# Optimization experiments

Hardware: AMD Instinct MI355X
Metric: run time of the kernel (lower is better)

## Reference

```python
import jax, jax.numpy as jnp
import numpy as np

NEG = -1e9  # large negative for masked logits (TRT uses dtype min)

def _rotate_every_two(x):
    # pairs (x0,x1) -> (-x1, x0), interleaved along last dim
    xr = x.reshape(*x.shape[:-1], -1, 2)
    rot = jnp.stack([-xr[..., 1], xr[..., 0]], axis=-1)
    return rot.reshape(x.shape)

def _apply_rope(x, cos, sin):
    # rot_dim == cos.shape[-1]; here it equals the full inner dim
    rot_dim = cos.shape[-1]
    x_rot, x_pass = x[..., :rot_dim], x[..., rot_dim:]
    x_rot = x_rot * cos + _rotate_every_two(x_rot) * sin
    return jnp.concatenate([x_rot, x_pass], axis=-1) if x_pass.shape[-1] else x_rot

def setup_inputs() -> dict:
    key = jax.random.key(0)
    ks = jax.random.split(key, 12)
    B, N, D_MODEL, H, DH = 2, 2048, 1024, 16, 64
    INNER = H * DH
    x = jax.random.normal(ks[0], (B, N, D_MODEL), dtype=jnp.float32)
    # rope angles: build realistic cos/sin tables repeated per head
    pos = jnp.arange(N, dtype=jnp.float32)
    inv = 1.0 / (10000.0 ** (jnp.arange(0, DH, 2, dtype=jnp.float32) / DH))
    ang = pos[:, None] * inv[None, :]              # [N, DH/2]
    ang = jnp.repeat(ang, 2, axis=-1)              # [N, DH] interleaved pairs
    ang = jnp.tile(ang, (1, H))                    # [N, INNER]
    rope_cos = jnp.broadcast_to(jnp.cos(ang)[None], (B, N, INNER)).astype(jnp.float32)
    rope_sin = jnp.broadcast_to(jnp.sin(ang)[None], (B, N, INNER)).astype(jnp.float32)
    input_lengths = jax.random.randint(ks[1], (B,), N // 2, N + 1, dtype=jnp.int32)
    s = 1.0 / np.sqrt(D_MODEL)
    Wq = jax.random.normal(ks[2], (D_MODEL, INNER), dtype=jnp.float32) * s
    bq = jnp.zeros((INNER,), jnp.float32)
    Wk = jax.random.normal(ks[3], (D_MODEL, INNER), dtype=jnp.float32) * s
    bk = jnp.zeros((INNER,), jnp.float32)
    Wv = jax.random.normal(ks[4], (D_MODEL, INNER), dtype=jnp.float32) * s
    bv = jnp.zeros((INNER,), jnp.float32)
    Wo = jax.random.normal(ks[5], (INNER, D_MODEL), dtype=jnp.float32) * (1.0 / np.sqrt(INNER))
    bo = jnp.zeros((D_MODEL,), jnp.float32)
    return {"x": x, "rope_cos": rope_cos, "rope_sin": rope_sin,
            "input_lengths": input_lengths,
            "Wq": Wq, "bq": bq, "Wk": Wk, "bk": bk, "Wv": Wv, "bv": bv,
            "Wo": Wo, "bo": bo}

def reference(x, rope_cos, rope_sin, input_lengths, Wq, bq, Wk, bk, Wv, bv, Wo, bo):
    B, N, _ = x.shape
    H, DH = 16, 64
    q = x @ Wq + bq
    k = x @ Wk + bk
    v = x @ Wv + bv
    q = _apply_rope(q, rope_cos, rope_sin)
    k = _apply_rope(k, rope_cos, rope_sin)
    # split heads: [B,N,H,DH] -> [B,H,N,DH]
    q = q.reshape(B, N, H, DH).transpose(0, 2, 1, 3)
    k = k.reshape(B, N, H, DH).transpose(0, 2, 1, 3)
    v = v.reshape(B, N, H, DH).transpose(0, 2, 1, 3)
    # NOTE: faithful to the non-plugin source path, q is NOT pre-scaled
    scores = jnp.einsum('bhqd,bhkd->bhqk', q, k)
    key_mask = jnp.arange(N)[None, :] < input_lengths[:, None]  # [B,N]
    scores = scores + jnp.where(key_mask, 0.0, NEG).astype(scores.dtype)[:, None, None, :]
    probs = jax.nn.softmax(scores, axis=-1)
    ctx = jnp.einsum('bhqk,bhkd->bhqd', probs, v)  # [B,H,N,DH]
    ctx = ctx.transpose(0, 2, 1, 3).reshape(B, N, H * DH)
    out = ctx @ Wo + bo
    out = out * key_mask[..., None].astype(out.dtype)
    return out
```

## Files before the change

kernel.cpp:

```cpp
#include <hip/hip_runtime.h>
#include <hip/hip_bf16.h>


typedef __fp16 fp16x2 __attribute__((ext_vector_type(2)));
typedef _Float16 f16x8 __attribute__((ext_vector_type(8)));
typedef float f32x4 __attribute__((ext_vector_type(4)));
typedef float f32x16 __attribute__((ext_vector_type(16)));

#define NEGBIG (-1.0e9f)

__device__ inline f32x4 mfma16(f16x8 a, f16x8 b, f32x4 c) {
  return __builtin_amdgcn_mfma_f32_16x16x32_f16(a, b, c, 0, 0, 0);
}
__device__ inline f32x16 mfma32(f16x8 a, f16x8 b, f32x16 c) {
  return __builtin_amdgcn_mfma_f32_32x32x16_f16(a, b, c, 0, 0, 0);
}

__device__ inline void gload16(const void* g, void* l) {
  __builtin_amdgcn_global_load_lds(
      (const __attribute__((address_space(1))) void*)g,
      (__attribute__((address_space(3))) void*)l, 16, 0, 0);
}

__device__ inline unsigned pk2u(float a, float b) {
  union { fp16x2 h; unsigned u; } x;
  x.h = __builtin_amdgcn_cvt_pkrtz(a, b);
  return x.u;
}

__device__ inline float max3f(float a, float b, float c) {
  float d;
  asm("v_max3_f32 %0, %1, %2, %3" : "=v"(d) : "v"(a), "v"(b), "v"(c));
  return d;
}

__global__ __launch_bounds__(256) void prep_kernel(
    const float* __restrict__ x, const float* __restrict__ Wq,
    const float* __restrict__ Wk, const float* __restrict__ Wv,
    const float* __restrict__ Wo, const float* __restrict__ rc,
    const float* __restrict__ rs, _Float16* __restrict__ xh,
    _Float16* __restrict__ wt, float* __restrict__ rc2,
    float* __restrict__ rs2) {
  __shared__ float tile[32][33];
  const int z = blockIdx.z;
  const int tx = threadIdx.x, ty = threadIdx.y;
  if (z == 4) {
    const int bid = blockIdx.y * 32 + blockIdx.x;
    const int t = ty * 32 + tx;
#pragma unroll
    for (int i = 0; i < 4; ++i) {
      const int o = bid * 1024 + i * 256 + t;
      const float4 v = ((const float4*)x)[o];
      union { _Float16 h[4]; short4 s; } u;
      u.h[0] = (_Float16)v.x; u.h[1] = (_Float16)v.y;
      u.h[2] = (_Float16)v.z; u.h[3] = (_Float16)v.w;
      ((short4*)xh)[o] = u.s;
    }
    return;
  }
  if (z == 5) {
    const int bid = blockIdx.y * 32 + blockIdx.x;
    const int idx = bid * 256 + ty * 32 + tx;
    if (idx < 131072) {
      const int n = idx >> 6, d = idx & 63;
      rc2[idx] = rc[(size_t)n * 1024 + d];
      rs2[idx] = rs[(size_t)n * 1024 + d];
    }
    return;
  }
  const float* W = (z == 0) ? Wq : (z == 1) ? Wk : (z == 2) ? Wv : Wo;
  _Float16* dh = wt + (size_t)z * 1024 * 1024;
  const int j0 = blockIdx.x * 32, k0 = blockIdx.y * 32;
  for (int i = ty; i < 32; i += 8)
    tile[i][tx] = W[(size_t)(k0 + i) * 1024 + j0 + tx];
  __syncthreads();
  for (int i = ty; i < 32; i += 8)
    dh[(size_t)(j0 + i) * 1024 + k0 + tx] = (_Float16)tile[tx][i];
}

template <int TM, int EPI>
__global__ __launch_bounds__(256) void gemm_kernel(
    const _Float16* __restrict__ A, const _Float16* __restrict__ B,
    const float* __restrict__ bias0, const float* __restrict__ bias1,
    const float* __restrict__ bias2,
    const float* __restrict__ ropeC, const float* __restrict__ ropeS,
    const int* __restrict__ lens,
    _Float16* __restrict__ outQK, _Float16* __restrict__ outVT,
    float* __restrict__ outF) {
  constexpr int MI = TM / 32;
  constexpr int MSHIFT = (TM == 128) ? 5 : 6;
  __shared__ __align__(16) _Float16 smem[(TM + 128) * 32];
  const int t = threadIdx.x;
  const int w = t >> 6, lane = t & 63;
  const int wr = w >> 1, wc = w & 1;
  const int fr = lane & 15, fg = lane >> 4;
  const int nwg = gridDim.x;
  const int bid = blockIdx.x;
  const int wgid = (bid & 7) * (nwg >> 3) + (bid >> 3);
  const int mtile = wgid & ((1 << MSHIFT) - 1);
  const int ntile = wgid >> MSHIFT;

  const int srow = t >> 2;
  const int skel = (t & 3) << 3;
  const size_t aBase = (size_t)(mtile * TM + srow) * 1024 + skel;
  const size_t bBase = (size_t)(ntile * 128 + srow) * 1024 + skel;
  const int ldst = t * 8;
  _Float16* lA = &smem[0];
  _Float16* lB = &smem[TM * 32];

  f32x4 acc[MI][4];
#pragma unroll
  for (int i = 0; i < MI; ++i)
#pragma unroll
    for (int j = 0; j < 4; ++j) {
      acc[i][j][0] = 0.f; acc[i][j][1] = 0.f; acc[i][j][2] = 0.f; acc[i][j][3] = 0.f;
    }

  for (int k0 = 0; k0 < 1024; k0 += 32) {
    gload16(A + aBase + k0, lA + ldst);
    if constexpr (TM == 128) gload16(A + aBase + k0 + 64 * 1024, lA + ldst + 2048);
    gload16(B + bBase + k0, lB + ldst);
    gload16(B + bBase + k0 + 64 * 1024, lB + ldst + 2048);
    __syncthreads();

    f16x8 af[MI], bf[4];
#pragma unroll
    for (int mi = 0; mi < MI; ++mi)
      af[mi] = *(const f16x8*)&lA[(wr * (TM / 2) + mi * 16 + fr) * 32 + fg * 8];
#pragma unroll
    for (int ni = 0; ni < 4; ++ni)
      bf[ni] = *(const f16x8*)&lB[(wc * 64 + ni * 16 + fr) * 32 + fg * 8];
#pragma unroll
    for (int mi = 0; mi < MI; ++mi)
#pragma unroll
      for (int ni = 0; ni < 4; ++ni)
        acc[mi][ni] = mfma16(af[mi], bf[ni], acc[mi][ni]);
    __syncthreads();
  }

  const int rowbase = mtile * TM + wr * (TM / 2);
  const int colbase = ntile * 128 + wc * 64;

  if constexpr (EPI == 0) {
    const int which = colbase >> 10;
    if (which < 2) {
      const float* bias = which ? bias1 : bias0;
      const int hh = (colbase >> 6) & 15;
      const int b = rowbase >> 11;
      const int nbase = rowbase & 2047;
      _Float16* lslab = smem + w * 1152;
      const char* cslab = (const char*)lslab;
      _Float16* qkbase =
          outQK + (size_t)((which * 2 + b) * 16 + hh) * 2048 * 64;
      const int rrow = lane >> 2;
      const int rqo = (lane & 3) * 32;
#pragma unroll
      for (int mi = 0; mi < MI; ++mi) {
#pragma unroll
        for (int ni = 0; ni < 4; ++ni) {
          const int dd = ni * 16 + fr;
          const float bv = bias[hh * 64 + dd];
#pragma unroll
          for (int r = 0; r < 4; ++r) {
            const int n = nbase + mi * 16 + fg * 4 + r;
            float val = acc[mi][ni][r] + bv;
            float part = __shfl_xor(val, 1);
            const int ro = n * 64 + dd;
            const float c = ropeC[ro], s = ropeS[ro];
            float rot = (fr & 1) ? (val * c + part * s) : (val * c - part * s);
            if (!which) rot *= 1.44269504f;
            lslab[(fg * 4 + r) * 72 + dd] = (_Float16)rot;
          }
        }
        asm volatile("" ::: "memory");
        const uint4 v0 = *(const uint4*)(cslab + rrow * 144 + rqo);
        const uint4 v1 = *(const uint4*)(cslab + rrow * 144 + rqo + 16);
        _Float16* gdst =
            qkbase + (size_t)(nbase + mi * 16 + rrow) * 64 + (lane & 3) * 16;
        *(uint4*)gdst = v0;
        *(uint4*)(gdst + 8) = v1;
        asm volatile("" ::: "memory");
      }
    } else {
#pragma unroll
      for (int ni = 0; ni < 4; ++ni) {
        const int gcol = colbase + ni * 16 + fr;
        const int jj = gcol & 1023;
        const int hh = jj >> 6, dd = jj & 63;
        const float bv = bias2[jj];
#pragma unroll
        for (int mi = 0; mi < MI; ++mi) {
          const int n0 = rowbase + mi * 16 + fg * 4;
          const int b = n0 >> 11, n = n0 & 2047;
          union { _Float16 h[4]; short4 s4; } u;
#pragma unroll
          for (int r = 0; r < 4; ++r) u.h[r] = (_Float16)(acc[mi][ni][r] + bv);
          *(short4*)(outVT + ((size_t)(b * 16 + hh) * 64 + dd) * 2048 + n) = u.s4;
        }
      }
    }
  } else {
    const int b = rowbase >> 11;
    const int len = lens[b];
#pragma unroll
    for (int ni = 0; ni < 4; ++ni) {
      const int gcol = colbase + ni * 16 + fr;
      const float bv = bias0[gcol];
#pragma unroll
      for (int mi = 0; mi < MI; ++mi) {
#pragma unroll
        for (int r = 0; r < 4; ++r) {
          const int m = rowbase + mi * 16 + fg * 4 + r;
          const int n = m & 2047;
          float val = acc[mi][ni][r] + bv;
          if (n >= len) val = 0.f;
          outF[(size_t)m * 1024 + gcol] = val;
        }
      }
    }
  }
}

__global__ __launch_bounds__(256, 4) void attn_kernel(
    const _Float16* __restrict__ qk, const _Float16* __restrict__ vt,
    const int* __restrict__ lens, unsigned* __restrict__ po,
    float2* __restrict__ ml) {
  __shared__ __align__(16) char lds[32768];
  const int t = threadIdx.x;
  const int w = t >> 6, lane = t & 63;
  const int lq = lane & 31, hi = lane >> 5;
  const int gid = blockIdx.x;
  const int xcd = gid & 7, idx = gid >> 3;
  const int qtile = idx & 15;
  const int c = ((idx >> 4) << 3) + xcd;
  const int bh = c >> 2, seg = c & 3;
  const int b = bh >> 4, h = bh & 15;
  const int len = lens[b];
  const int q0w = qtile * 128 + w * 32;
  const size_t qoff = (size_t)(b * 16 + h) * 2048 * 64;
  const size_t koff = (size_t)((2 + b) * 16 + h) * 2048 * 64;
  const size_t voff = (size_t)(b * 16 + h) * 64 * 2048;

  f16x8 qf[4];
#pragma unroll
  for (int ks = 0; ks < 4; ++ks)
    qf[ks] = *(const f16x8*)(qk + qoff + (size_t)(q0w + lq) * 64 + ks * 16 + hi * 8);

  const int srow = t >> 3;
  const int ss = (t & 7) ^ (srow & 7);
  const size_t kg = koff + (size_t)srow * 64 + ss * 8;
  const int vd = srow + ((ss >> 2) << 5);
  const size_t vg = voff + (size_t)vd * 2048 + (ss & 3) * 8;

  f32x16 o0, o1;
#pragma unroll
  for (int i = 0; i < 16; ++i) { o0[i] = 0.f; o1[i] = 0.f; }
  float mrun = 0.f, lsum = 0.f;

  fp16x2 ones2;
  ones2[0] = (__fp16)1.0f; ones2[1] = (__fp16)1.0f;

#define STAGE(bi, tile0) do { \
    char* dst = lds + (bi) * 16384 + t * 16; \
    const size_t kk = (size_t)(tile0) * 2048;  \
    gload16(qk + kg + kk, dst); \
    gload16(qk + kg + kk + 2048, dst + 4096); \
    gload16(vt + vg + (tile0) * 32, dst + 8192); \
    gload16(vt + vg + (tile0) * 32 + 32, dst + 12288); \
  } while (0)

  const int nkb = (len + 31) >> 5;
  const int tb0 = (nkb * seg) >> 2;
  const int tb1 = (nkb * (seg + 1)) >> 2;
  const int nst = (tb1 - tb0 + 1) >> 1;

  STAGE(0, tb0);

  for (int st = 0; st < nst; ++st) {
    const int cur = st & 1;
    if (st + 1 < nst) {
      STAGE(cur ^ 1, tb0 + (st + 1) * 2);
      asm volatile("s_waitcnt vmcnt(4)" ::: "memory");
    } else {
      asm volatile("s_waitcnt vmcnt(0)" ::: "memory");
    }
    __builtin_amdgcn_s_barrier();

    const char* Bb = lds + cur * 16384;
    const int rsw = (lq & 7) << 4;

#pragma unroll
    for (int ch = 0; ch < 2; ++ch) {
      const int kb = tb0 + st * 2 + ch;
      if (kb < tb1) {
        const char* Kb = Bb + ch * 4096;
        const char* Vb = Bb + 8192 + ch * 4096;

        f32x16 s0;
        const float nm = -mrun;
#pragma unroll
        for (int i = 0; i < 16; ++i) s0[i] = nm;
        __builtin_amdgcn_s_setprio(1);
#pragma unroll
        for (int ks = 0; ks < 4; ++ks) {
          const f16x8 kf =
              *(const f16x8*)(Kb + lq * 128 + ((ks * 32 + hi * 16) ^ rsw));
          s0 = mfma32(kf, qf[ks], s0);
        }
        __builtin_amdgcn_s_setprio(0);

        if (kb == nkb - 1 && (len & 31)) {
#pragma unroll
          for (int r = 0; r < 16; ++r) {
            const int key = kb * 32 + (r & 3) + ((r >> 2) << 3) + hi * 4;
            if (key >= len) s0[r] = NEGBIG;
          }
        }

        const float m0 = max3f(s0[0], s0[1], s0[2]);
        const float m1 = max3f(s0[3], s0[4], s0[5]);
        const float m2 = max3f(s0[6], s0[7], s0[8]);
        const float m3 = max3f(s0[9], s0[10], s0[11]);
        const float m4 = max3f(s0[12], s0[13], s0[14]);
        float mx = fmaxf(max3f(m0, m1, m2), max3f(m3, m4, s0[15]));
        mx = fmaxf(mx, __shfl_xor(mx, 32));

        const bool first = (kb == tb0);
        if (first || !__all(mx <= 8.f)) {
          const float delta = first ? mx : fmaxf(mx, 0.f);
          const float scq = __builtin_amdgcn_exp2f(-delta);
          mrun += delta;
          lsum *= scq;
          float sc[16];
#pragma unroll
          for (int r = 0; r < 16; ++r)
            sc[r] = __shfl(scq, (r & 3) + ((r >> 2) << 3) + hi * 4);
#pragma unroll
          for (int r = 0; r < 16; ++r) { o0[r] *= sc[r]; o1[r] *= sc[r]; }
#pragma unroll
          for (int i = 0; i < 16; ++i) s0[i] -= delta;
        }

        unsigned W[8];
#pragma unroll
        for (int u = 0; u < 4; ++u) {
          const float p0 = __builtin_amdgcn_exp2f(s0[4 * u + 0]);
          const float p1 = __builtin_amdgcn_exp2f(s0[4 * u + 1]);
          const float p2 = __builtin_amdgcn_exp2f(s0[4 * u + 2]);
          const float p3 = __builtin_amdgcn_exp2f(s0[4 * u + 3]);
          W[2 * u] = pk2u(p0, p1);
          W[2 * u + 1] = pk2u(p2, p3);
        }
        float ps = 0.f;
#pragma unroll
        for (int i = 0; i < 8; ++i) {
          union { unsigned u; fp16x2 h; } x; x.u = W[i];
          ps = __builtin_amdgcn_fdot2(x.h, ones2, ps, false);
        }
        ps += __shfl_xor(ps, 32);
        lsum += ps;

        __builtin_amdgcn_s_setprio(1);
#pragma unroll
        for (int ks = 0; ks < 2; ++ks) {
          const unsigned w0 = W[4 * ks + 0], w1 = W[4 * ks + 1];
          const unsigned w2 = W[4 * ks + 2], w3 = W[4 * ks + 3];
          const unsigned sendA = hi ? w0 : w2;
          const unsigned sendB = hi ? w1 : w3;
          const unsigned recvA = __shfl_xor(sendA, 32);
          const unsigned recvB = __shfl_xor(sendB, 32);
          union { unsigned u[4]; f16x8 v; } af;
          af.u[0] = hi ? recvA : w0;
          af.u[1] = hi ? recvB : w1;
          af.u[2] = hi ? w2 : recvA;
          af.u[3] = hi ? w3 : recvB;
          const int g0 = ks * 2 + hi;
          const f16x8 v0f = *(const f16x8*)(Vb + lq * 128 + ((g0 << 4) ^ rsw));
          const f16x8 v1f =
              *(const f16x8*)(Vb + lq * 128 + (((g0 + 4) << 4) ^ rsw));
          o0 = mfma32(af.v, v0f, o0);
          o1 = mfma32(af.v, v1f, o1);
        }
        __builtin_amdgcn_s_setprio(0);
      }
    }

    asm volatile("" ::: "memory");
    __builtin_amdgcn_s_barrier();
  }
#undef STAGE

  const size_t rowbase = (size_t)bh * 2048 + q0w;
  const float li = 1.f / lsum;
  unsigned* pod = po + ((size_t)seg * 65536 + rowbase) * 32;
#pragma unroll
  for (int r = 0; r < 16; ++r) {
    const int qr = (r & 3) + ((r >> 2) << 3) + hi * 4;
    const float lr = __shfl(li, qr);
    pod[qr * 32 + lq] = pk2u(o0[r] * lr, o1[r] * lr);
  }
  if (hi == 0) {
    float2 v; v.x = mrun; v.y = lsum;
    ml[(size_t)seg * 65536 + rowbase + lq] = v;
  }
}

__global__ __launch_bounds__(256) void combine_kernel(
    const unsigned* __restrict__ po, const float2* __restrict__ ml,
    _Float16* __restrict__ ctx) {
  const int tid = blockIdx.x * 256 + threadIdx.x;
  const int row = tid >> 5, dg = tid & 31;
  const float2 a0 = ml[row];
  const float2 a1 = ml[65536 + row];
  const float2 a2 = ml[131072 + row];
  const float2 a3 = ml[196608 + row];
  const float m = fmaxf(fmaxf(a0.x, a1.x), fmaxf(a2.x, a3.x));
  const float w0 = a0.y * __builtin_amdgcn_exp2f(a0.x - m);
  const float w1 = a1.y * __builtin_amdgcn_exp2f(a1.x - m);
  const float w2 = a2.y * __builtin_amdgcn_exp2f(a2.x - m);
  const float w3 = a3.y * __builtin_amdgcn_exp2f(a3.x - m);
  const float inv = 1.f / (w0 + w1 + w2 + w3);
  float acc0 = 0.f, acc1 = 0.f;
  const float f[4] = {w0 * inv, w1 * inv, w2 * inv, w3 * inv};
#pragma unroll
  for (int s = 0; s < 4; ++s) {
    union { unsigned u; fp16x2 h; } x;
    x.u = po[((size_t)s * 65536 + row) * 32 + dg];
    acc0 += f[s] * (float)x.h[0];
    acc1 += f[s] * (float)x.h[1];
  }
  const int bh = row >> 11, n = row & 2047, b = bh >> 4, h = bh & 15;
  _Float16* dst = ctx + ((size_t)(b * 2048 + n) * 1024 + h * 64);
  dst[dg] = (_Float16)acc0;
  dst[dg + 32] = (_Float16)acc1;
}


extern "C" void kernel_launch(void* const* d_in, const int* in_sizes, int n_in,
                              void* d_out, int out_size, void* d_ws, size_t ws_size,
                              hipStream_t stream) {
  const float* x = (const float*)d_in[0];
  const float* rc = (const float*)d_in[1];
  const float* rs = (const float*)d_in[2];
  const int* lens = (const int*)d_in[3];
  const float* Wq = (const float*)d_in[4];
  const float* bq = (const float*)d_in[5];
  const float* Wk = (const float*)d_in[6];
  const float* bk = (const float*)d_in[7];
  const float* Wv = (const float*)d_in[8];
  const float* bv = (const float*)d_in[9];
  const float* Wo = (const float*)d_in[10];
  const float* bo = (const float*)d_in[11];
  float* out = (float*)d_out;

  char* ws = (char*)d_ws;
  const size_t MB = 1024 * 1024;
  _Float16* XH = (_Float16*)(ws + 0);
  _Float16* WT = (_Float16*)(ws + 8 * MB);
  _Float16* QK = (_Float16*)(ws + 16 * MB);
  _Float16* VT = (_Float16*)(ws + 32 * MB);
  _Float16* CTX = (_Float16*)(ws + 40 * MB);
  unsigned* PO = (unsigned*)(ws + 48 * MB);
  float2* ML = (float2*)(ws + 80 * MB);
  float* RC2 = (float*)(ws + 48 * MB);
  float* RS2 = (float*)(ws + 48 * MB + 512 * 1024);

  prep_kernel<<<dim3(32, 32, 6), dim3(32, 8), 0, stream>>>(
      x, Wq, Wk, Wv, Wo, rc, rs, XH, WT, RC2, RS2);
  gemm_kernel<128, 0><<<768, 256, 0, stream>>>(
      XH, WT, bq, bk, bv, RC2, RS2, nullptr, QK, VT, nullptr);
  attn_kernel<<<2048, 256, 0, stream>>>(QK, VT, lens, PO, ML);
  combine_kernel<<<8192, 256, 0, stream>>>(PO, ML, CTX);
  gemm_kernel<64, 2><<<512, 256, 0, stream>>>(
      CTX, WT + (size_t)3 * 1024 * 1024, bo, nullptr, nullptr, nullptr,
      nullptr, lens, nullptr, nullptr, out);
}
```

Baseline: 152.8 us.

## Replace QKV projection GEMM with 256x256-tile 512-thread kernel

Adds a dedicated QKV projection kernel that uses 256x256 output tiles, 512 threads, a BK=64 double-buffered LDS pipeline with XOR swizzle and direct global-to-LDS loads, and MFMA priority raising. The launch drops from 768 blocks to 192. The goal is more operand reuse per byte loaded and less LDS traffic than the 128x128 tiles. In exchange it uses 128 KB of LDS and large accumulator register files, so occupancy is one block per CU, and 192 blocks may underfill the 256 CUs. The old templated GEMM is reduced to the output-projection epilogue.

```diff
diff --git a/kernel.cpp b/kernel.cpp
--- a/kernel.cpp
+++ b/kernel.cpp
@@ -78,14 +78,151 @@
     dh[(size_t)(j0 + i) * 1024 + k0 + tx] = (_Float16)tile[tx][i];
 }
 
+__global__ __launch_bounds__(512) void gemm256_kernel(
+    const _Float16* __restrict__ A, const _Float16* __restrict__ B,
+    const float* __restrict__ bias0, const float* __restrict__ bias1,
+    const float* __restrict__ bias2, const float* __restrict__ ropeC,
+    const float* __restrict__ ropeS, _Float16* __restrict__ outQK,
+    _Float16* __restrict__ outVT) {
+  __shared__ __align__(16) char lds[131072];
+  const int t = threadIdx.x;
+  const int lane = t & 63, w = t >> 6;
+  const int wr = w >> 2, wc = w & 3;
+  const int fr = lane & 15, fg = lane >> 4;
+  const int bid = blockIdx.x;
+  const int wgid = (bid & 7) * 24 + (bid >> 3);
+  const int mtile = wgid & 15, ntile = wgid >> 4;
+
+  const int srw = t >> 3;
+  const int ss8 = (((t & 7) ^ (srw & 7)) << 3);
+  const size_t aRow = (size_t)(mtile * 256 + srw) * 1024 + ss8;
+  const size_t bRow = (size_t)(ntile * 256 + srw) * 1024 + ss8;
+  const int t16 = t * 16;
+
+  f32x4 acc[8][4];
+#pragma unroll
+  for (int i = 0; i < 8; ++i)
+#pragma unroll
+    for (int j = 0; j < 4; ++j) {
+      acc[i][j][0] = 0.f; acc[i][j][1] = 0.f; acc[i][j][2] = 0.f; acc[i][j][3] = 0.f;
+    }
+
+#define G256(c, kt_) do { \
+    const size_t kc = (size_t)(kt_) * 64; \
+    char* ab = lds + (c) * 32768 + t16; \
+    char* bb = lds + 65536 + (c) * 32768 + t16; \
+    gload16(A + aRow + kc, ab); \
+    gload16(A + aRow + kc + 65536, ab + 8192); \
+    gload16(A + aRow + kc + 131072, ab + 16384); \
+    gload16(A + aRow + kc + 196608, ab + 24576); \
+    gload16(B + bRow + kc, bb); \
+    gload16(B + bRow + kc + 65536, bb + 8192); \
+    gload16(B + bRow + kc + 131072, bb + 16384); \
+    gload16(B + bRow + kc + 196608, bb + 24576); \
+  } while (0)
+
+  G256(0, 0);
+  for (int kt = 0; kt < 16; ++kt) {
+    const int cur = kt & 1;
+    if (kt < 15) {
+      G256(cur ^ 1, kt + 1);
+      asm volatile("s_waitcnt vmcnt(8)" ::: "memory");
+    } else {
+      asm volatile("s_waitcnt vmcnt(0)" ::: "memory");
+    }
+    __builtin_amdgcn_s_barrier();
+
+    const char* La = lds + cur * 32768;
+    const char* Lb = lds + 65536 + cur * 32768;
+    const int swz = (fr & 7) << 4;
+#pragma unroll
+    for (int kk = 0; kk < 2; ++kk) {
+      const int ko = (kk * 64 + fg * 16) ^ swz;
+      f16x8 af[8], bf[4];
+#pragma unroll
+      for (int mi = 0; mi < 8; ++mi)
+        af[mi] = *(const f16x8*)(La + (wr * 128 + mi * 16 + fr) * 128 + ko);
+#pragma unroll
+      for (int ni = 0; ni < 4; ++ni)
+        bf[ni] = *(const f16x8*)(Lb + (wc * 64 + ni * 16 + fr) * 128 + ko);
+      __builtin_amdgcn_s_setprio(1);
+#pragma unroll
+      for (int mi = 0; mi < 8; ++mi)
+#pragma unroll
+        for (int ni = 0; ni < 4; ++ni)
+          acc[mi][ni] = mfma16(af[mi], bf[ni], acc[mi][ni]);
+      __builtin_amdgcn_s_setprio(0);
+    }
+    asm volatile("" ::: "memory");
+    __builtin_amdgcn_s_barrier();
+  }
+#undef G256
+
+  const int rowbase = mtile * 256 + wr * 128;
+  const int colbase = ntile * 256 + wc * 64;
+  const int which = colbase >> 10;
+
+  if (which < 2) {
+    const float* bias = which ? bias1 : bias0;
+    const int hh = (colbase >> 6) & 15;
+    const int b = rowbase >> 11;
+    const int nbase = rowbase & 2047;
+    _Float16* lslab = (_Float16*)lds + w * 1152;
+    const char* cslab = (const char*)lslab;
+    _Float16* qkbase = outQK + (size_t)((which * 2 + b) * 16 + hh) * 2048 * 64;
+    const int rrow = lane >> 2;
+    const int rqo = (lane & 3) * 32;
+#pragma unroll
+    for (int mi = 0; mi < 8; ++mi) {
+#pragma unroll
+      for (int ni = 0; ni < 4; ++ni) {
+        const int dd = ni * 16 + fr;
+        const float bv = bias[hh * 64 + dd];
+#pragma unroll
+        for (int r = 0; r < 4; ++r) {
+          const int n = nbase + mi * 16 + fg * 4 + r;
+          float val = acc[mi][ni][r] + bv;
+          float part = __shfl_xor(val, 1);
+          const int ro = n * 64 + dd;
+          const float c = ropeC[ro], s = ropeS[ro];
+          float rot = (fr & 1) ? (val * c + part * s) : (val * c - part * s);
+          if (!which) rot *= 1.44269504f;
+          lslab[(fg * 4 + r) * 72 + dd] = (_Float16)rot;
+        }
+      }
+      asm volatile("" ::: "memory");
+      const uint4 v0 = *(const uint4*)(cslab + rrow * 144 + rqo);
+      const uint4 v1 = *(const uint4*)(cslab + rrow * 144 + rqo + 16);
+      _Float16* gdst =
+          qkbase + (size_t)(nbase + mi * 16 + rrow) * 64 + (lane & 3) * 16;
+      *(uint4*)gdst = v0;
+      *(uint4*)(gdst + 8) = v1;
+      asm volatile("" ::: "memory");
+    }
+  } else {
+#pragma unroll
+    for (int ni = 0; ni < 4; ++ni) {
+      const int gcol = colbase + ni * 16 + fr;
+      const int jj = gcol & 1023;
+      const int hh = jj >> 6, dd = jj & 63;
+      const float bv = bias2[jj];
+#pragma unroll
+      for (int mi = 0; mi < 8; ++mi) {
+        const int n0 = rowbase + mi * 16 + fg * 4;
+        const int b = n0 >> 11, n = n0 & 2047;
+        union { _Float16 h[4]; short4 s4; } u;
+#pragma unroll
+        for (int r = 0; r < 4; ++r) u.h[r] = (_Float16)(acc[mi][ni][r] + bv);
+        *(short4*)(outVT + ((size_t)(b * 16 + hh) * 64 + dd) * 2048 + n) = u.s4;
+      }
+    }
+  }
+}
+
 template <int TM, int EPI>
 __global__ __launch_bounds__(256) void gemm_kernel(
     const _Float16* __restrict__ A, const _Float16* __restrict__ B,
-    const float* __restrict__ bias0, const float* __restrict__ bias1,
-    const float* __restrict__ bias2,
-    const float* __restrict__ ropeC, const float* __restrict__ ropeS,
-    const int* __restrict__ lens,
-    _Float16* __restrict__ outQK, _Float16* __restrict__ outVT,
+    const float* __restrict__ bias0, const int* __restrict__ lens,
     float* __restrict__ outF) {
   constexpr int MI = TM / 32;
   constexpr int MSHIFT = (TM == 128) ? 5 : 6;
@@ -140,82 +277,21 @@
 
   const int rowbase = mtile * TM + wr * (TM / 2);
   const int colbase = ntile * 128 + wc * 64;
-
-  if constexpr (EPI == 0) {
-    const int which = colbase >> 10;
-    if (which < 2) {
-      const float* bias = which ? bias1 : bias0;
-      const int hh = (colbase >> 6) & 15;
-      const int b = rowbase >> 11;
-      const int nbase = rowbase & 2047;
-      _Float16* lslab = smem + w * 1152;
-      const char* cslab = (const char*)lslab;
-      _Float16* qkbase =
-          outQK + (size_t)((which * 2 + b) * 16 + hh) * 2048 * 64;
-      const int rrow = lane >> 2;
-      const int rqo = (lane & 3) * 32;
-#pragma unroll
-      for (int mi = 0; mi < MI; ++mi) {
-#pragma unroll
-        for (int ni = 0; ni < 4; ++ni) {
-          const int dd = ni * 16 + fr;
-          const float bv = bias[hh * 64 + dd];
-#pragma unroll
-          for (int r = 0; r < 4; ++r) {
-            const int n = nbase + mi * 16 + fg * 4 + r;
-            float val = acc[mi][ni][r] + bv;
-            float part = __shfl_xor(val, 1);
-            const int ro = n * 64 + dd;
-            const float c = ropeC[ro], s = ropeS[ro];
-            float rot = (fr & 1) ? (val * c + part * s) : (val * c - part * s);
-            if (!which) rot *= 1.44269504f;
-            lslab[(fg * 4 + r) * 72 + dd] = (_Float16)rot;
-          }
-        }
-        asm volatile("" ::: "memory");
-        const uint4 v0 = *(const uint4*)(cslab + rrow * 144 + rqo);
-        const uint4 v1 = *(const uint4*)(cslab + rrow * 144 + rqo + 16);
-        _Float16* gdst =
-            qkbase + (size_t)(nbase + mi * 16 + rrow) * 64 + (lane & 3) * 16;
-        *(uint4*)gdst = v0;
-        *(uint4*)(gdst + 8) = v1;
-        asm volatile("" ::: "memory");
-      }
-    } else {
-#pragma unroll
-      for (int ni = 0; ni < 4; ++ni) {
-        const int gcol = colbase + ni * 16 + fr;
-        const int jj = gcol & 1023;
-        const int hh = jj >> 6, dd = jj & 63;
-        const float bv = bias2[jj];
-#pragma unroll
-        for (int mi = 0; mi < MI; ++mi) {
-          const int n0 = rowbase + mi * 16 + fg * 4;
-          const int b = n0 >> 11, n = n0 & 2047;
-          union { _Float16 h[4]; short4 s4; } u;
-#pragma unroll
-          for (int r = 0; r < 4; ++r) u.h[r] = (_Float16)(acc[mi][ni][r] + bv);
-          *(short4*)(outVT + ((size_t)(b * 16 + hh) * 64 + dd) * 2048 + n) = u.s4;
-        }
-      }
-    }
-  } else {
-    const int b = rowbase >> 11;
-    const int len = lens[b];
-#pragma unroll
-    for (int ni = 0; ni < 4; ++ni) {
-      const int gcol = colbase + ni * 16 + fr;
-      const float bv = bias0[gcol];
-#pragma unroll
-      for (int mi = 0; mi < MI; ++mi) {
-#pragma unroll
-        for (int r = 0; r < 4; ++r) {
-          const int m = rowbase + mi * 16 + fg * 4 + r;
-          const int n = m & 2047;
-          float val = acc[mi][ni][r] + bv;
-          if (n >= len) val = 0.f;
-          outF[(size_t)m * 1024 + gcol] = val;
-        }
+  const int b = rowbase >> 11;
+  const int len = lens[b];
+#pragma unroll
+  for (int ni = 0; ni < 4; ++ni) {
+    const int gcol = colbase + ni * 16 + fr;
+    const float bv = bias0[gcol];
+#pragma unroll
+    for (int mi = 0; mi < MI; ++mi) {
+#pragma unroll
+      for (int r = 0; r < 4; ++r) {
+        const int m = rowbase + mi * 16 + fg * 4 + r;
+        const int n = m & 2047;
+        float val = acc[mi][ni][r] + bv;
+        if (n >= len) val = 0.f;
+        outF[(size_t)m * 1024 + gcol] = val;
       }
     }
   }
@@ -262,7 +338,7 @@
 
 #define STAGE(bi, tile0) do { \
     char* dst = lds + (bi) * 16384 + t * 16; \
-    const size_t kk = (size_t)(tile0) * 2048;  \
+    const size_t kk = (size_t)(tile0) * 2048; \
     gload16(qk + kg + kk, dst); \
     gload16(qk + kg + kk + 2048, dst + 4096); \
     gload16(vt + vg + (tile0) * 32, dst + 8192); \
@@ -467,11 +543,10 @@
 
   prep_kernel<<<dim3(32, 32, 6), dim3(32, 8), 0, stream>>>(
       x, Wq, Wk, Wv, Wo, rc, rs, XH, WT, RC2, RS2);
-  gemm_kernel<128, 0><<<768, 256, 0, stream>>>(
-      XH, WT, bq, bk, bv, RC2, RS2, nullptr, QK, VT, nullptr);
+  gemm256_kernel<<<192, 512, 0, stream>>>(XH, WT, bq, bk, bv, RC2, RS2, QK,
+                                          VT);
   attn_kernel<<<2048, 256, 0, stream>>>(QK, VT, lens, PO, ML);
   combine_kernel<<<8192, 256, 0, stream>>>(PO, ML, CTX);
   gemm_kernel<64, 2><<<512, 256, 0, stream>>>(
-      CTX, WT + (size_t)3 * 1024 * 1024, bo, nullptr, nullptr, nullptr,
-      nullptr, lens, nullptr, nullptr, out);
-}
+      CTX, WT + (size_t)3 * 1024 * 1024, bo, lens, out);
+}
```

Result: faster. 138.2 us (-9.5%).
